# Performance work log

Hardware: AMD Instinct MI355X
Metric: run time of the kernel (lower is better)

Reference implementation:

```python
import jax, jax.numpy as jnp
import numpy as np

B, D, C, K = 8192, 2048, 4096, 1000  # batch, input_dim, num_centers, num_classes


def setup_inputs() -> dict:
    key = jax.random.key(0)
    k0, k1, k2 = jax.random.split(key, 3)
    x = jax.random.normal(k0, (B, D), dtype=jnp.float32)
    centers = jax.random.normal(k1, (C, D), dtype=jnp.float32)
    beta = jnp.ones((C,), dtype=jnp.float32)
    W = jax.random.normal(k2, (K, C), dtype=jnp.float32) * 0.02  # fc.weight
    b = jnp.zeros((K,), dtype=jnp.float32)  # fc.bias
    return {"x": x, "centers": centers, "beta": beta, "W": W, "b": b}


def reference(x, centers, beta, W, b):
    # Pairwise Euclidean distance via the Gram trick (same math as
    # torch.norm(x[:,None,:] - centers, dim=2), without the (B,C,D) intermediate).
    x2 = jnp.sum(x * x, axis=-1, keepdims=True)          # (B, 1)
    c2 = jnp.sum(centers * centers, axis=-1)             # (C,)
    sq = x2 + c2[None, :] - 2.0 * (x @ centers.T)        # (B, C) squared distances
    dist = jnp.sqrt(jnp.maximum(sq, 0.0))
    act = jnp.exp(-beta[None, :] * dist)                 # RBF activations
    act = act / jnp.sum(act, axis=1, keepdims=True)      # normalize over centers
    return act @ W.T + b                                 # linear head (B, K)
```

## Files before the change

kernel.cpp:

```cpp
#include <hip/hip_runtime.h>


#define BB 8192
#define DD 2048
#define CC 4096
#define KK 1000
#define KP 1024

typedef unsigned short u16;
typedef __bf16 bf16x8 __attribute__((ext_vector_type(8)));
typedef float f32x4 __attribute__((ext_vector_type(4)));

typedef const void __attribute__((address_space(1)))* gvp_t;
typedef void __attribute__((address_space(3)))* lvp_t;

__device__ __forceinline__ u16 f2bf(float f) {
  union { float f; unsigned u; } v; v.f = f;
  return (u16)((v.u + 0x7fffu + ((v.u >> 16) & 1u)) >> 16);
}

__global__ void prep_norm_cast(const float* __restrict__ x, const float* __restrict__ cen,
                               u16* __restrict__ xb, u16* __restrict__ cb,
                               float* __restrict__ x2, float* __restrict__ c2,
                               float* __restrict__ rowsum) {
  int row = blockIdx.x;
  const float* src;
  u16* dst;
  float* nrm;
  if (row < BB) {
    src = x + (size_t)row * DD; dst = xb + (size_t)row * DD; nrm = x2 + row;
  } else {
    int r = row - BB;
    src = cen + (size_t)r * DD; dst = cb + (size_t)r * DD; nrm = c2 + r;
  }
  int t = threadIdx.x;
  if (row < BB && t == 0) rowsum[row] = 0.f;
  float s = 0.f;
#pragma unroll
  for (int m = 0; m < 2; ++m) {
    int idx = t + 256 * m;
    float4 v = reinterpret_cast<const float4*>(src)[idx];
    s += v.x * v.x + v.y * v.y + v.z * v.z + v.w * v.w;
    reinterpret_cast<ushort4*>(dst)[idx] =
        make_ushort4(f2bf(v.x), f2bf(v.y), f2bf(v.z), f2bf(v.w));
  }
#pragma unroll
  for (int off = 1; off < 64; off <<= 1) s += __shfl_xor(s, off);
  __shared__ float red[4];
  if ((t & 63) == 0) red[t >> 6] = s;
  __syncthreads();
  if (t == 0) *nrm = red[0] + red[1] + red[2] + red[3];
}

__global__ void prep_wcast(const float* __restrict__ W, u16* __restrict__ wb) {
  int row = blockIdx.x;
  int t = threadIdx.x;
  ushort4* dst = reinterpret_cast<ushort4*>(wb + (size_t)row * CC);
  if (row < KK) {
    const float4* src = reinterpret_cast<const float4*>(W + (size_t)row * CC);
#pragma unroll
    for (int m = 0; m < 4; ++m) {
      float4 v = src[t + 256 * m];
      dst[t + 256 * m] = make_ushort4(f2bf(v.x), f2bf(v.y), f2bf(v.z), f2bf(v.w));
    }
  } else {
#pragma unroll
    for (int m = 0; m < 4; ++m) dst[t + 256 * m] = make_ushort4(0, 0, 0, 0);
  }
}

#define SB0 __builtin_amdgcn_sched_barrier(0)
#define BARR __builtin_amdgcn_s_barrier()
#define LGKM0 asm volatile("s_waitcnt lgkmcnt(0)" ::: "memory")


#define ST_A(BUF, H, TILE)                                                         \
  {                                                                                \
    const u16* _s = gA0 + (size_t)((H) * 128) * DD + (TILE) * 64;                  \
    char* _d = (char*)smem + (BUF) * 65536 + (H) * 16384 + t * 16;                 \
    __builtin_amdgcn_global_load_lds((gvp_t)_s, (lvp_t)_d, 16, 0, 0);              \
    __builtin_amdgcn_global_load_lds((gvp_t)(_s + (size_t)64 * DD),                \
                                     (lvp_t)(_d + 8192), 16, 0, 0);                \
  }

#define ST_B(BUF, H, TILE)                                                         \
  {                                                                                \
    const u16* _s = gB0 + (size_t)((H) * 128) * DD + (TILE) * 64;                  \
    char* _d = (char*)smem + (BUF) * 65536 + 32768 + (H) * 16384 + t * 16;         \
    __builtin_amdgcn_global_load_lds((gvp_t)_s, (lvp_t)_d, 16, 0, 0);              \
    __builtin_amdgcn_global_load_lds((gvp_t)(_s + (size_t)64 * DD),                \
                                     (lvp_t)(_d + 8192), 16, 0, 0);                \
  }

#define READ_B(SBP)                                                                \
  _Pragma("unroll") for (int n_ = 0; n_ < 4; ++n_) {                               \
    _Pragma("unroll") for (int ks_ = 0; ks_ < 2; ++ks_) {                          \
      bfr[n_][ks_] = *(const bf16x8*)((SBP) + bRow + n_ * 2048 + cbv[ks_]);        \
    }                                                                              \
  }

#define READ_A(SAP, MQ)                                                            \
  _Pragma("unroll") for (int m_ = 0; m_ < 2; ++m_) {                               \
    _Pragma("unroll") for (int ks_ = 0; ks_ < 2; ++ks_) {                          \
      af[m_][ks_] =                                                                \
          *(const bf16x8*)((SAP) + aRow + ((MQ)*2 + m_) * 2048 + cbv[ks_]);        \
    }                                                                              \
  }

#define MFMA_Q(MQ)                                                                 \
  __builtin_amdgcn_s_setprio(1);                                                   \
  _Pragma("unroll") for (int m_ = 0; m_ < 2; ++m_) {                               \
    _Pragma("unroll") for (int n_ = 0; n_ < 4; ++n_) {                             \
      _Pragma("unroll") for (int ks_ = 0; ks_ < 2; ++ks_) {                        \
        acc[(MQ)*2 + m_][n_] = __builtin_amdgcn_mfma_f32_16x16x32_bf16(            \
            af[m_][ks_], bfr[n_][ks_], acc[(MQ)*2 + m_][n_], 0, 0, 0);             \
      }                                                                            \
    }                                                                              \
  }                                                                                \
  __builtin_amdgcn_s_setprio(0)

#define TILE_BODY(TILE, CUR, DOA, DOB, VMN)                                        \
  {                                                                                \
    const char* sA_ = (const char*)smem + (CUR) * 65536;                           \
    const char* sB_ = sA_ + 32768;                                                 \
    READ_B(sB_);                                                                   \
    READ_A(sA_, 0);                                                                \
    SB0;                                                                           \
    if (DOA) { ST_A(1 - (CUR), 0, (TILE) + 1); ST_A(1 - (CUR), 1, (TILE) + 1); }   \
    SB0; BARR; LGKM0; SB0;                                                         \
    MFMA_Q(0); SB0; BARR;                                                          \
    READ_A(sA_, 1); SB0;                                                           \
    if (DOB) { ST_B((CUR), 0, (TILE) + 2); }                                       \
    SB0; BARR; LGKM0; SB0;                                                         \
    MFMA_Q(1); SB0; BARR;                                                          \
    READ_A(sA_, 2); SB0;                                                           \
    if (DOB) { ST_B((CUR), 1, (TILE) + 2); }                                       \
    SB0; BARR; LGKM0; SB0;                                                         \
    MFMA_Q(2); SB0; BARR;                                                          \
    READ_A(sA_, 3); SB0; BARR; LGKM0; SB0;                                         \
    MFMA_Q(3);                                                                     \
    if ((VMN) == 4) { asm volatile("s_waitcnt vmcnt(4)" ::: "memory"); }           \
    else if ((VMN) == 0) { asm volatile("s_waitcnt vmcnt(0)" ::: "memory"); }      \
    SB0; BARR;                                                                     \
  }

__global__ __launch_bounds__(512, 2)
void gemm1_rbf(const u16* __restrict__ Abf, const u16* __restrict__ Bbf,
               const float* __restrict__ x2, const float* __restrict__ c2,
               const float* __restrict__ beta, u16* __restrict__ Ebf,
               float* __restrict__ rowsum) {
  constexpr int NT = DD / 64;
  __shared__ __align__(16) char smem[131072];

  const int t = threadIdx.x;
  const int lane = t & 63;
  const int wave = t >> 6;
  const int wr = wave >> 2;
  const int wc = wave & 3;
  const int l15 = lane & 15;

  const int rowBase = blockIdx.y * 256;
  const int colBase = blockIdx.x * 256;

  f32x4 acc[8][4];
#pragma unroll
  for (int i = 0; i < 8; ++i)
#pragma unroll
    for (int j = 0; j < 4; ++j) acc[i][j] = 0.f;

  const int srow = t >> 3;
  const u16* gA0 = Abf + (size_t)(rowBase + srow) * DD + ((t & 7) ^ (srow & 7)) * 8;
  const u16* gB0 = Bbf + (size_t)(colBase + srow) * DD + ((t & 7) ^ (srow & 7)) * 8;

  int cbv[2];
  cbv[0] = (((lane >> 4) & 3) ^ (lane & 7)) << 4;
  cbv[1] = ((4 + ((lane >> 4) & 3)) ^ (lane & 7)) << 4;
  const int aRow = (wr * 128 + l15) * 128;
  const int bRow = (wc * 64 + l15) * 128;

  bf16x8 bfr[4][2];
  bf16x8 af[2][2];

  ST_A(0, 0, 0); ST_A(0, 1, 0); ST_B(0, 0, 0); ST_B(0, 1, 0);
  ST_B(1, 0, 1); ST_B(1, 1, 1);
  asm volatile("s_waitcnt vmcnt(4)" ::: "memory");
  BARR;

#pragma unroll 2
  for (int tile = 0; tile < NT - 2; ++tile) {
    TILE_BODY(tile, tile & 1, true, true, 4);
  }
  TILE_BODY(NT - 2, (NT - 2) & 1, true, false, 0);
  TILE_BODY(NT - 1, (NT - 1) & 1, false, false, -1);

  const int khi4 = (lane >> 4) * 4;
  float c2v[4], bet[4];
  int gc[4];
#pragma unroll
  for (int n = 0; n < 4; ++n) {
    gc[n] = colBase + wc * 64 + n * 16 + l15;
    c2v[n] = c2[gc[n]];
    bet[n] = beta[gc[n]];
  }
#pragma unroll
  for (int m = 0; m < 8; ++m) {
#pragma unroll
    for (int r = 0; r < 4; ++r) {
      const int grow = rowBase + wr * 128 + m * 16 + khi4 + r;
      const float x2v = x2[grow];
      u16* orow = Ebf + (size_t)grow * CC;
      float rs = 0.f;
#pragma unroll
      for (int n = 0; n < 4; ++n) {
        float d = acc[m][n][r];
        float sq = fmaxf(x2v + c2v[n] - 2.0f * d, 0.0f);
        float e = __expf(-bet[n] * __builtin_amdgcn_sqrtf(sq));
        rs += e;
        orow[gc[n]] = f2bf(e);
      }
#pragma unroll
      for (int off = 1; off < 16; off <<= 1) rs += __shfl_xor(rs, off);
      if (l15 == 0) atomicAdd(&rowsum[grow], rs);
    }
  }
}


#define ST2_A(BUF, H, TILE)                                                        \
  {                                                                                \
    const u16* _s = gA0 + (size_t)((H) * 128) * CC + (TILE) * 64;                  \
    char* _d = (char*)smem + (BUF) * 49152 + (H) * 16384 + t * 16;                 \
    __builtin_amdgcn_global_load_lds((gvp_t)_s, (lvp_t)_d, 16, 0, 0);              \
    __builtin_amdgcn_global_load_lds((gvp_t)(_s + (size_t)64 * CC),                \
                                     (lvp_t)(_d + 8192), 16, 0, 0);                \
  }

#define ST2_B(BUF, TILE)                                                           \
  {                                                                                \
    const u16* _s = gB0 + (TILE) * 64;                                             \
    char* _d = (char*)smem + (BUF) * 49152 + 32768 + t * 16;                       \
    __builtin_amdgcn_global_load_lds((gvp_t)_s, (lvp_t)_d, 16, 0, 0);              \
    __builtin_amdgcn_global_load_lds((gvp_t)(_s + (size_t)64 * CC),                \
                                     (lvp_t)(_d + 8192), 16, 0, 0);                \
  }

#define READ2_B(SBP)                                                               \
  _Pragma("unroll") for (int n_ = 0; n_ < 2; ++n_) {                               \
    _Pragma("unroll") for (int ks_ = 0; ks_ < 2; ++ks_) {                          \
      bfr[n_][ks_] = *(const bf16x8*)((SBP) + bRow + n_ * 2048 + cbv[ks_]);        \
    }                                                                              \
  }

#define READ2_A(SAP, MQ)                                                           \
  _Pragma("unroll") for (int m_ = 0; m_ < 2; ++m_) {                               \
    _Pragma("unroll") for (int ks_ = 0; ks_ < 2; ++ks_) {                          \
      af[m_][ks_] =                                                                \
          *(const bf16x8*)((SAP) + aRow + ((MQ)*2 + m_) * 2048 + cbv[ks_]);        \
    }                                                                              \
  }

#define MFMA2_Q(MQ)                                                                \
  __builtin_amdgcn_s_setprio(1);                                                   \
  _Pragma("unroll") for (int m_ = 0; m_ < 2; ++m_) {                               \
    _Pragma("unroll") for (int n_ = 0; n_ < 2; ++n_) {                             \
      _Pragma("unroll") for (int ks_ = 0; ks_ < 2; ++ks_) {                        \
        acc[(MQ)*2 + m_][n_] = __builtin_amdgcn_mfma_f32_16x16x32_bf16(            \
            af[m_][ks_], bfr[n_][ks_], acc[(MQ)*2 + m_][n_], 0, 0, 0);             \
      }                                                                            \
    }                                                                              \
  }                                                                                \
  __builtin_amdgcn_s_setprio(0)

#define TILE2_BODY(TILE, CUR, DOA, DOB, VMN)                                       \
  {                                                                                \
    const char* sA_ = (const char*)smem + (CUR) * 49152;                           \
    const char* sB_ = sA_ + 32768;                                                 \
    READ2_B(sB_);                                                                  \
    READ2_A(sA_, 0);                                                               \
    SB0;                                                                           \
    if (DOA) { ST2_A(1 - (CUR), 0, (TILE) + 1); }                                  \
    SB0; BARR; LGKM0; SB0;                                                         \
    MFMA2_Q(0); SB0; BARR;                                                         \
    READ2_A(sA_, 1); SB0;                                                          \
    if (DOA) { ST2_A(1 - (CUR), 1, (TILE) + 1); }                                  \
    SB0; BARR; LGKM0; SB0;                                                         \
    MFMA2_Q(1); SB0; BARR;                                                         \
    READ2_A(sA_, 2); SB0;                                                          \
    if (DOB) { ST2_B((CUR), (TILE) + 2); }                                         \
    SB0; BARR; LGKM0; SB0;                                                         \
    MFMA2_Q(2); SB0; BARR;                                                         \
    READ2_A(sA_, 3); SB0; BARR; LGKM0; SB0;                                        \
    MFMA2_Q(3);                                                                    \
    if ((VMN) == 2) { asm volatile("s_waitcnt vmcnt(2)" ::: "memory"); }           \
    else if ((VMN) == 0) { asm volatile("s_waitcnt vmcnt(0)" ::: "memory"); }      \
    SB0; BARR;                                                                     \
  }

__global__ __launch_bounds__(512, 2)
void gemm2_out(const u16* __restrict__ Ebf, const u16* __restrict__ Wbf,
               const float* __restrict__ rowsum, const float* __restrict__ bias,
               float* __restrict__ out) {
  constexpr int NT = CC / 64;
  __shared__ __align__(16) char smem[98304];

  const int t = threadIdx.x;
  const int lane = t & 63;
  const int wave = t >> 6;
  const int wr = wave >> 2;
  const int wc = wave & 3;
  const int l15 = lane & 15;

  const int rowBase = blockIdx.y * 256;
  const int colBase = blockIdx.x * 128;

  f32x4 acc[8][2];
#pragma unroll
  for (int i = 0; i < 8; ++i)
#pragma unroll
    for (int j = 0; j < 2; ++j) acc[i][j] = 0.f;

  const int srow = t >> 3;
  const u16* gA0 = Ebf + (size_t)(rowBase + srow) * CC + ((t & 7) ^ (srow & 7)) * 8;
  const u16* gB0 = Wbf + (size_t)(colBase + srow) * CC + ((t & 7) ^ (srow & 7)) * 8;

  int cbv[2];
  cbv[0] = (((lane >> 4) & 3) ^ (lane & 7)) << 4;
  cbv[1] = ((4 + ((lane >> 4) & 3)) ^ (lane & 7)) << 4;
  const int aRow = (wr * 128 + l15) * 128;
  const int bRow = (wc * 32 + l15) * 128;

  bf16x8 bfr[2][2];
  bf16x8 af[2][2];

  ST2_A(0, 0, 0); ST2_A(0, 1, 0); ST2_B(0, 0);
  ST2_B(1, 1);
  asm volatile("s_waitcnt vmcnt(2)" ::: "memory");
  BARR;

#pragma unroll 2
  for (int tile = 0; tile < NT - 2; ++tile) {
    TILE2_BODY(tile, tile & 1, true, true, 2);
  }
  TILE2_BODY(NT - 2, (NT - 2) & 1, true, false, 0);
  TILE2_BODY(NT - 1, (NT - 1) & 1, false, false, -1);

  const int khi4 = (lane >> 4) * 4;
  int gc[2];
  float bv[2];
#pragma unroll
  for (int n = 0; n < 2; ++n) {
    gc[n] = colBase + wc * 32 + n * 16 + l15;
    bv[n] = (gc[n] < KK) ? bias[gc[n]] : 0.f;
  }
#pragma unroll
  for (int m = 0; m < 8; ++m) {
#pragma unroll
    for (int r = 0; r < 4; ++r) {
      const int grow = rowBase + wr * 128 + m * 16 + khi4 + r;
      const float inv = 1.0f / rowsum[grow];
#pragma unroll
      for (int n = 0; n < 2; ++n) {
        if (gc[n] < KK)
          out[(size_t)grow * KK + gc[n]] = acc[m][n][r] * inv + bv[n];
      }
    }
  }
}

#define OFF_XB 0u
#define OFF_CB 33554432u
#define OFF_WB 50331648u
#define OFF_EB 58720256u
#define OFF_X2 125829120u
#define OFF_C2 125861888u
#define OFF_RS 125878272u

extern "C" void kernel_launch(void* const* d_in, const int* in_sizes, int n_in,
                              void* d_out, int out_size, void* d_ws, size_t ws_size,
                              hipStream_t stream) {
  const float* x = (const float*)d_in[0];
  const float* cen = (const float*)d_in[1];
  const float* beta = (const float*)d_in[2];
  const float* W = (const float*)d_in[3];
  const float* bias = (const float*)d_in[4];
  float* out = (float*)d_out;
  char* ws = (char*)d_ws;

  u16* xb = (u16*)(ws + OFF_XB);
  u16* cb = (u16*)(ws + OFF_CB);
  u16* wb = (u16*)(ws + OFF_WB);
  u16* eb = (u16*)(ws + OFF_EB);
  float* x2 = (float*)(ws + OFF_X2);
  float* c2 = (float*)(ws + OFF_C2);
  float* rowsum = (float*)(ws + OFF_RS);

  prep_norm_cast<<<BB + CC, 256, 0, stream>>>(x, cen, xb, cb, x2, c2, rowsum);
  prep_wcast<<<KP, 256, 0, stream>>>(W, wb);
  gemm1_rbf<<<dim3(CC / 256, BB / 256), 512, 0, stream>>>(xb, cb, x2, c2, beta, eb, rowsum);
  gemm2_out<<<dim3(KP / 128, BB / 256), 512, 0, stream>>>(eb, wb, rowsum, bias, out);
}
```

Baseline: 377.8 us.

## Compute row sums via MFMA in gemm2 and merge prep kernels

Drops the per-row atomicAdd reduction of the RBF activations from the gemm1 epilogue. Each row sum is instead computed inside gemm2 by extra MFMAs against a vector of bf16 ones, reusing the A fragments already loaded from LDS. The two prep kernels are merged into one launch. This removes the atomics and the rowsum traffic, at the cost of extra MFMA work per tile in gemm2, which is repeated across every column block. The sums now come from the bf16-rounded activations rather than fp32 values.

```diff
diff --git a/kernel.cpp b/kernel.cpp
--- a/kernel.cpp
+++ b/kernel.cpp
@@ -19,11 +19,29 @@
   return (u16)((v.u + 0x7fffu + ((v.u >> 16) & 1u)) >> 16);
 }
 
-__global__ void prep_norm_cast(const float* __restrict__ x, const float* __restrict__ cen,
-                               u16* __restrict__ xb, u16* __restrict__ cb,
-                               float* __restrict__ x2, float* __restrict__ c2,
-                               float* __restrict__ rowsum) {
+__global__ void prep_all(const float* __restrict__ x, const float* __restrict__ cen,
+                         const float* __restrict__ W,
+                         u16* __restrict__ xb, u16* __restrict__ cb,
+                         u16* __restrict__ wb,
+                         float* __restrict__ x2, float* __restrict__ c2) {
   int row = blockIdx.x;
+  int t = threadIdx.x;
+  if (row >= BB + CC) {
+    int r = row - BB - CC;
+    ushort4* dst = reinterpret_cast<ushort4*>(wb + (size_t)r * CC);
+    if (r < KK) {
+      const float4* src = reinterpret_cast<const float4*>(W + (size_t)r * CC);
+#pragma unroll
+      for (int m = 0; m < 4; ++m) {
+        float4 v = src[t + 256 * m];
+        dst[t + 256 * m] = make_ushort4(f2bf(v.x), f2bf(v.y), f2bf(v.z), f2bf(v.w));
+      }
+    } else {
+#pragma unroll
+      for (int m = 0; m < 4; ++m) dst[t + 256 * m] = make_ushort4(0, 0, 0, 0);
+    }
+    return;
+  }
   const float* src;
   u16* dst;
   float* nrm;
@@ -33,8 +51,6 @@
     int r = row - BB;
     src = cen + (size_t)r * DD; dst = cb + (size_t)r * DD; nrm = c2 + r;
   }
-  int t = threadIdx.x;
-  if (row < BB && t == 0) rowsum[row] = 0.f;
   float s = 0.f;
 #pragma unroll
   for (int m = 0; m < 2; ++m) {
@@ -50,23 +66,6 @@
   if ((t & 63) == 0) red[t >> 6] = s;
   __syncthreads();
   if (t == 0) *nrm = red[0] + red[1] + red[2] + red[3];
-}
-
-__global__ void prep_wcast(const float* __restrict__ W, u16* __restrict__ wb) {
-  int row = blockIdx.x;
-  int t = threadIdx.x;
-  ushort4* dst = reinterpret_cast<ushort4*>(wb + (size_t)row * CC);
-  if (row < KK) {
-    const float4* src = reinterpret_cast<const float4*>(W + (size_t)row * CC);
-#pragma unroll
-    for (int m = 0; m < 4; ++m) {
-      float4 v = src[t + 256 * m];
-      dst[t + 256 * m] = make_ushort4(f2bf(v.x), f2bf(v.y), f2bf(v.z), f2bf(v.w));
-    }
-  } else {
-#pragma unroll
-    for (int m = 0; m < 4; ++m) dst[t + 256 * m] = make_ushort4(0, 0, 0, 0);
-  }
 }
 
 #define SB0 __builtin_amdgcn_sched_barrier(0)
@@ -147,8 +146,7 @@
 __global__ __launch_bounds__(512, 2)
 void gemm1_rbf(const u16* __restrict__ Abf, const u16* __restrict__ Bbf,
                const float* __restrict__ x2, const float* __restrict__ c2,
-               const float* __restrict__ beta, u16* __restrict__ Ebf,
-               float* __restrict__ rowsum) {
+               const float* __restrict__ beta, u16* __restrict__ Ebf) {
   constexpr int NT = DD / 64;
   __shared__ __align__(16) char smem[131072];
 
@@ -209,18 +207,13 @@
       const int grow = rowBase + wr * 128 + m * 16 + khi4 + r;
       const float x2v = x2[grow];
       u16* orow = Ebf + (size_t)grow * CC;
-      float rs = 0.f;
 #pragma unroll
       for (int n = 0; n < 4; ++n) {
         float d = acc[m][n][r];
         float sq = fmaxf(x2v + c2v[n] - 2.0f * d, 0.0f);
         float e = __expf(-bet[n] * __builtin_amdgcn_sqrtf(sq));
-        rs += e;
         orow[gc[n]] = f2bf(e);
       }
-#pragma unroll
-      for (int off = 1; off < 16; off <<= 1) rs += __shfl_xor(rs, off);
-      if (l15 == 0) atomicAdd(&rowsum[grow], rs);
     }
   }
 }
@@ -269,6 +262,12 @@
       }                                                                            \
     }                                                                              \
   }                                                                                \
+  _Pragma("unroll") for (int m_ = 0; m_ < 2; ++m_) {                               \
+    _Pragma("unroll") for (int ks_ = 0; ks_ < 2; ++ks_) {                          \
+      rsacc[(MQ)*2 + m_] = __builtin_amdgcn_mfma_f32_16x16x32_bf16(                \
+          af[m_][ks_], onesf, rsacc[(MQ)*2 + m_], 0, 0, 0);                        \
+    }                                                                              \
+  }                                                                                \
   __builtin_amdgcn_s_setprio(0)
 
 #define TILE2_BODY(TILE, CUR, DOA, DOB, VMN)                                       \
@@ -298,8 +297,7 @@
 
 __global__ __launch_bounds__(512, 2)
 void gemm2_out(const u16* __restrict__ Ebf, const u16* __restrict__ Wbf,
-               const float* __restrict__ rowsum, const float* __restrict__ bias,
-               float* __restrict__ out) {
+               const float* __restrict__ bias, float* __restrict__ out) {
   constexpr int NT = CC / 64;
   __shared__ __align__(16) char smem[98304];
 
@@ -319,6 +317,13 @@
 #pragma unroll
     for (int j = 0; j < 2; ++j) acc[i][j] = 0.f;
 
+  f32x4 rsacc[8];
+#pragma unroll
+  for (int i = 0; i < 8; ++i) rsacc[i] = 0.f;
+  bf16x8 onesf;
+#pragma unroll
+  for (int e = 0; e < 8; ++e) onesf[e] = (__bf16)1.0f;
+
   const int srow = t >> 3;
   const u16* gA0 = Ebf + (size_t)(rowBase + srow) * CC + ((t & 7) ^ (srow & 7)) * 8;
   const u16* gB0 = Wbf + (size_t)(colBase + srow) * CC + ((t & 7) ^ (srow & 7)) * 8;
@@ -357,7 +362,7 @@
 #pragma unroll
     for (int r = 0; r < 4; ++r) {
       const int grow = rowBase + wr * 128 + m * 16 + khi4 + r;
-      const float inv = 1.0f / rowsum[grow];
+      const float inv = 1.0f / rsacc[m][r];
 #pragma unroll
       for (int n = 0; n < 2; ++n) {
         if (gc[n] < KK)
@@ -373,7 +378,6 @@
 #define OFF_EB 58720256u
 #define OFF_X2 125829120u
 #define OFF_C2 125861888u
-#define OFF_RS 125878272u
 
 extern "C" void kernel_launch(void* const* d_in, const int* in_sizes, int n_in,
                               void* d_out, int out_size, void* d_ws, size_t ws_size,
@@ -392,10 +396,8 @@
   u16* eb = (u16*)(ws + OFF_EB);
   float* x2 = (float*)(ws + OFF_X2);
   float* c2 = (float*)(ws + OFF_C2);
-  float* rowsum = (float*)(ws + OFF_RS);
-
-  prep_norm_cast<<<BB + CC, 256, 0, stream>>>(x, cen, xb, cb, x2, c2, rowsum);
-  prep_wcast<<<KP, 256, 0, stream>>>(W, wb);
-  gemm1_rbf<<<dim3(CC / 256, BB / 256), 512, 0, stream>>>(xb, cb, x2, c2, beta, eb, rowsum);
-  gemm2_out<<<dim3(KP / 128, BB / 256), 512, 0, stream>>>(eb, wb, rowsum, bias, out);
+
+  prep_all<<<BB + CC + KP, 256, 0, stream>>>(x, cen, W, xb, cb, wb, x2, c2);
+  gemm1_rbf<<<dim3(CC / 256, BB / 256), 512, 0, stream>>>(xb, cb, x2, c2, beta, eb);
+  gemm2_out<<<dim3(KP / 128, BB / 256), 512, 0, stream>>>(eb, wb, bias, out);
 }
```

Measured after the change: 354.5 us. 1.07x faster.
